# Performance work log

Hardware: AMD Instinct MI355X
Metric: run time of the kernel (lower is better)

The kernel has to match this reference:

```python
import jax, jax.numpy as jnp
import numpy as np

B, N, H, D = 1, 4096, 16, 64
C = H * D  # 1024
SCALE = D ** -0.5


def setup_inputs() -> dict:
    key = jax.random.key(0)
    k1, k2, k3, k4 = jax.random.split(key, 4)
    x = jax.random.normal(k1, (B, N, C), dtype=jnp.float32)
    # torch nn.Linear weights: [out_features, in_features]; y = x @ W.T + b
    w_qkv = jax.random.normal(k2, (3 * C, C), dtype=jnp.float32) * 0.02
    w_proj = jax.random.normal(k3, (C, C), dtype=jnp.float32) * 0.02
    b_proj = jax.random.normal(k4, (C,), dtype=jnp.float32) * 0.02
    return {"x": x, "w_qkv": w_qkv, "w_proj": w_proj, "b_proj": b_proj}


def reference(x, w_qkv, w_proj, b_proj):
    Bn, Nn, Cn = x.shape
    # fused QKV projection (no bias)
    qkv = jnp.einsum('bnc,oc->bno', x, w_qkv)            # [B,N,3C]
    qkv = qkv.reshape(Bn, Nn, 3, H, D)
    q = jnp.transpose(qkv[:, :, 0], (0, 2, 1, 3))        # [B,H,N,D]
    k = jnp.transpose(qkv[:, :, 1], (0, 2, 1, 3))
    v = jnp.transpose(qkv[:, :, 2], (0, 2, 1, 3))
    attn = jnp.einsum('bhnd,bhmd->bhnm', q, k) * SCALE   # [B,H,N,N]
    causal_mask = jnp.triu(jnp.ones((Nn, Nn), dtype=bool), k=1)
    attn = jnp.where(causal_mask, -jnp.inf, attn)
    attn = jax.nn.softmax(attn, axis=-1)
    out = jnp.einsum('bhnm,bhmd->bhnd', attn, v)          # [B,H,N,D]
    out = jnp.transpose(out, (0, 2, 1, 3)).reshape(Bn, Nn, Cn)
    out = jnp.einsum('bnc,oc->bno', out, w_proj) + b_proj
    return out
```

## Files before the change

kernel.cpp:

```cpp
#include <hip/hip_runtime.h>
#include <hip/hip_bf16.h>
#include <stdint.h>
#include <stddef.h>

using bf16 = __hip_bfloat16;
typedef short short8 __attribute__((ext_vector_type(8)));
typedef short short4v __attribute__((ext_vector_type(4)));
typedef short short2v __attribute__((ext_vector_type(2)));
typedef float f32x4 __attribute__((ext_vector_type(4)));
typedef float f32x16 __attribute__((ext_vector_type(16)));
typedef unsigned uintv4 __attribute__((ext_vector_type(4)));

#define MFMA16(A, B, C) __builtin_amdgcn_mfma_f32_16x16x32_bf16(A, B, C, 0, 0, 0)
#define MFMA32(A, B, C) __builtin_amdgcn_mfma_f32_32x32x16_bf16(A, B, C, 0, 0, 0)
#define GLOAD_LDS(g, l) __builtin_amdgcn_global_load_lds( \
    (const __attribute__((address_space(1))) void*)(g),   \
    (__attribute__((address_space(3))) void*)(l), 16, 0, 0)

constexpr int AN  = 4096;
constexpr int NH  = 16;
constexpr int HD  = 64;
constexpr int CC  = 1024;
constexpr int C3  = 3072;
constexpr float QSCALE = 0.125f * 1.4426950408889634f;

__device__ inline short bf16s(float f) {
    return (short)((__float_as_uint(f) + 0x8000u) >> 16);
}
__device__ inline float bf2f(short s) {
    return __uint_as_float(((unsigned)(unsigned short)s) << 16);
}
__device__ inline bf16 sbf(short s) {
    union { short s; bf16 b; } u;
    u.s = s;
    return u.b;
}
#if __has_builtin(__builtin_amdgcn_cvt_pk_bf16_f32)
typedef __bf16 bf16x2 __attribute__((ext_vector_type(2)));
__device__ inline short2v pk2(float a, float b) {
    bf16x2 r = __builtin_amdgcn_cvt_pk_bf16_f32(a, b);
    return *(short2v*)&r;
}
#else
__device__ inline short2v pk2(float a, float b) {
    unsigned ua = __float_as_uint(a) + 0x8000u;
    unsigned ub = __float_as_uint(b) + 0x8000u;
    unsigned r  = __builtin_amdgcn_perm(ub, ua, 0x07060302);
    return *(short2v*)&r;
}
#endif
__device__ inline unsigned pk2u(float a, float b) {
    short2v p = pk2(a, b);
    return *(unsigned*)&p;
}
__device__ inline short4v pack4(float a, float b, float c, float d) {
    short2v lo = pk2(a, b), hi = pk2(c, d);
    short4v r;
    r[0] = lo[0]; r[1] = lo[1]; r[2] = hi[0]; r[3] = hi[1];
    return r;
}
__device__ inline void plswap(unsigned &a, unsigned &b) {
    asm("v_permlane32_swap_b32 %0, %1" : "+v"(a), "+v"(b));
}
#if __has_builtin(__builtin_amdgcn_exp2f)
#define FAST_EXP2(x) __builtin_amdgcn_exp2f(x)
#else
#define FAST_EXP2(x) exp2f(x)
#endif

__device__ inline int detect_mode_inline(const unsigned short* xraw, int lane) {
    int crazy = 0;
    #pragma unroll
    for (int i = 0; i < 4; ++i) {
        const unsigned short u = xraw[lane * 4 + i];
        const int e = (u >> 7) & 0xFF;
        if (e >= 134 || (e != 0 && e <= 110)) ++crazy;
    }
    #pragma unroll
    for (int off = 32; off > 0; off >>= 1)
        crazy += __shfl_down(crazy, off, 64);
    crazy = __shfl(crazy, 0, 64);
    return (crazy >= 8) ? 1 : 0;
}

__device__ inline void cast8(const void* __restrict__ src,
                             bf16* __restrict__ dst, int i, int m) {
    if (m) {
        const float* s = (const float*)src;
        float4 a = *(const float4*)(s + i);
        float4 b = *(const float4*)(s + i + 4);
        short8 o;
        short2v p0 = pk2(a.x, a.y), p1 = pk2(a.z, a.w);
        short2v p2 = pk2(b.x, b.y), p3 = pk2(b.z, b.w);
        o[0] = p0[0]; o[1] = p0[1]; o[2] = p1[0]; o[3] = p1[1];
        o[4] = p2[0]; o[5] = p2[1]; o[6] = p3[0]; o[7] = p3[1];
        *(short8*)(dst + i) = o;
    } else {
        *(short8*)(dst + i) = *(const short8*)((const short*)src + i);
    }
}

__global__ void cast_all(const void* __restrict__ x, const void* __restrict__ wq,
                         const void* __restrict__ wp, const void* __restrict__ bp,
                         bf16* __restrict__ xb, bf16* __restrict__ wqb,
                         bf16* __restrict__ wpb, float* __restrict__ biasf,
                         int* __restrict__ mode) {
    const int b = blockIdx.x;
    const int tid = threadIdx.x;
    const int m = detect_mode_inline((const unsigned short*)x, tid & 63);
    if (b < 2048) {
        cast8(x, xb, (b * 256 + tid) * 8, m);
    } else if (b < 3584) {
        cast8(wq, wqb, ((b - 2048) * 256 + tid) * 8, m);
    } else if (b < 4096) {
        cast8(wp, wpb, ((b - 3584) * 256 + tid) * 8, m);
    } else {
        #pragma unroll
        for (int i = tid; i < CC; i += 256)
            biasf[i] = m ? ((const float*)bp)[i] : bf2f(((const short*)bp)[i]);
        if (tid == 0) *mode = m;
    }
}

constexpr int BM = 128, BN = 128, BK = 32;

__global__ __launch_bounds__(256, 3) void gemm_qkv(
    const bf16* __restrict__ A, const bf16* __restrict__ Bw,
    bf16* __restrict__ Cout, bf16* __restrict__ vTout)
{
    __shared__ bf16 As[BM * BK];
    __shared__ bf16 Bs[BN * BK];

    const int tid  = threadIdx.x;
    const int wave = tid >> 6;
    const int lane = tid & 63;
    const int quad = lane >> 4;
    const int l16  = lane & 15;
    const int wr   = wave >> 1;
    const int wc   = wave & 1;
    const int m0   = blockIdx.y * BM;
    const int o0   = blockIdx.x * BN;

    const int srow = lane >> 2;
    const int scol = (lane & 3) * 8;

    f32x4 acc[4][4] = {};

    for (int k0 = 0; k0 < CC; k0 += BK) {
        __syncthreads();
        #pragma unroll
        for (int c = 0; c < 2; ++c) {
            const int rbase = wave * 32 + c * 16;
            GLOAD_LDS(A + (size_t)(m0 + rbase + srow) * CC + k0 + scol, &As[rbase * BK]);
            GLOAD_LDS(Bw + (size_t)(o0 + rbase + srow) * CC + k0 + scol, &Bs[rbase * BK]);
        }
        __syncthreads();

        short8 af[4], bfr[4];
        #pragma unroll
        for (int i = 0; i < 4; ++i)
            af[i] = *(const short8*)&As[(wr * 64 + i * 16 + l16) * BK + quad * 8];
        #pragma unroll
        for (int j = 0; j < 4; ++j)
            bfr[j] = *(const short8*)&Bs[(wc * 64 + j * 16 + l16) * BK + quad * 8];
        #pragma unroll
        for (int i = 0; i < 4; ++i)
            #pragma unroll
            for (int j = 0; j < 4; ++j)
                acc[i][j] = MFMA16(af[i], bfr[j], acc[i][j]);
    }

    if (o0 >= 2 * CC) {
        #pragma unroll
        for (int j = 0; j < 4; ++j) {
            const int vc = o0 - 2 * CC + wc * 64 + j * 16 + l16;
            #pragma unroll
            for (int i = 0; i < 4; ++i) {
                const int row0 = m0 + wr * 64 + i * 16 + quad * 4;
                *(short4v*)&vTout[(size_t)vc * AN + row0] =
                    pack4(acc[i][j][0], acc[i][j][1], acc[i][j][2], acc[i][j][3]);
            }
        }
        return;
    }
    const float qs = (o0 < CC) ? QSCALE : 1.0f;
    #pragma unroll
    for (int j = 0; j < 4; ++j) {
        const int col = o0 + wc * 64 + j * 16 + l16;
        #pragma unroll
        for (int i = 0; i < 4; ++i) {
            const int row = m0 + wr * 64 + i * 16 + quad * 4;
            #pragma unroll
            for (int r = 0; r < 2; ++r) {
                short2v p = pk2(acc[i][j][2 * r] * qs, acc[i][j][2 * r + 1] * qs);
                Cout[(size_t)(row + 2 * r) * C3 + col]     = sbf(p[0]);
                Cout[(size_t)(row + 2 * r + 1) * C3 + col] = sbf(p[1]);
            }
        }
    }
}

constexpr int PM = 128, PN = 64, PK = 32;

__global__ __launch_bounds__(256, 2) void gemm_proj(
    const bf16* __restrict__ A, const bf16* __restrict__ Bw,
    const float* __restrict__ bias, void* __restrict__ Cout,
    const int* __restrict__ mode)
{
    __shared__ bf16 As[PM * PK];
    __shared__ bf16 Bs[PN * PK];

    const int tid  = threadIdx.x;
    const int wave = tid >> 6;
    const int lane = tid & 63;
    const int quad = lane >> 4;
    const int l16  = lane & 15;
    const int wr   = wave >> 1;
    const int wc   = wave & 1;
    const int m0   = blockIdx.y * PM;
    const int o0   = blockIdx.x * PN;
    const bool f32out = (*mode != 0);

    const int srow = lane >> 2;
    const int scol = (lane & 3) * 8;

    f32x4 acc[4][2] = {};

    for (int k0 = 0; k0 < CC; k0 += PK) {
        __syncthreads();
        #pragma unroll
        for (int c = 0; c < 2; ++c) {
            const int rbase = wave * 32 + c * 16;
            GLOAD_LDS(A + (size_t)(m0 + rbase + srow) * CC + k0 + scol, &As[rbase * PK]);
        }
        {
            const int rbase = wave * 16;
            GLOAD_LDS(Bw + (size_t)(o0 + rbase + srow) * CC + k0 + scol, &Bs[rbase * PK]);
        }
        __syncthreads();

        short8 af[4], bfr[2];
        #pragma unroll
        for (int i = 0; i < 4; ++i)
            af[i] = *(const short8*)&As[(wr * 64 + i * 16 + l16) * PK + quad * 8];
        #pragma unroll
        for (int j = 0; j < 2; ++j)
            bfr[j] = *(const short8*)&Bs[(wc * 32 + j * 16 + l16) * PK + quad * 8];
        #pragma unroll
        for (int i = 0; i < 4; ++i)
            #pragma unroll
            for (int j = 0; j < 2; ++j)
                acc[i][j] = MFMA16(af[i], bfr[j], acc[i][j]);
    }

    #pragma unroll
    for (int j = 0; j < 2; ++j) {
        const int col = o0 + wc * 32 + j * 16 + l16;
        const float bv = bias[col];
        #pragma unroll
        for (int i = 0; i < 4; ++i) {
            const int row = m0 + wr * 64 + i * 16 + quad * 4;
            if (f32out) {
                #pragma unroll
                for (int r = 0; r < 4; ++r)
                    ((float*)Cout)[(size_t)(row + r) * CC + col] = acc[i][j][r] + bv;
            } else {
                #pragma unroll
                for (int r = 0; r < 2; ++r) {
                    short2v p = pk2(acc[i][j][2 * r] + bv, acc[i][j][2 * r + 1] + bv);
                    ((bf16*)Cout)[(size_t)(row + 2 * r) * CC + col]     = sbf(p[0]);
                    ((bf16*)Cout)[(size_t)(row + 2 * r + 1) * CC + col] = sbf(p[1]);
                }
            }
        }
    }
}

constexpr int TK = 64;

__global__ __launch_bounds__(128, 2) void attn6(
    const bf16* __restrict__ qkv, const bf16* __restrict__ vT,
    bf16* __restrict__ pOn, float* __restrict__ pl)
{
    __shared__ bf16 Ks[2][TK * HD];
    __shared__ bf16 Vs[2][HD * TK];

    const int tid  = threadIdx.x;
    const int wave = tid >> 6;
    const int lane = tid & 63;
    const int l31  = lane & 31;
    const int hh   = lane >> 5;
    const int h7   = l31 & 7;
    const int h    = blockIdx.x & 15;
    const int t    = blockIdx.x >> 4;

    short8 ones8;
    #pragma unroll
    for (int i = 0; i < 8; ++i) ones8[i] = (short)0x3F80;

    const int sr  = lane >> 3;
    const int pc  = lane & 7;
    const int swz = pc ^ (sr & 7);

    #pragma unroll 1
    for (int pp = 0; pp < 2; ++pp) {
        const int tile = pp ? 63 - t : t;
        const int nIt  = tile + 1;
        const int i0   = pp ? ((64 - t) + 1) >> 1 : 0;
        const int i1   = pp ? 64 - t : (t + 2) >> 1;
        const int half = pp;
        const int qw   = tile * 64 + wave * 32;
        const int q    = qw + l31;

        short8 qf[4];
        {
            const bf16* qp = qkv + (size_t)q * C3 + h * HD + hh * 8;
            #pragma unroll
            for (int ki = 0; ki < 4; ++ki)
                qf[ki] = *(const short8*)(qp + ki * 16);
        }

        f32x16 acc_l = {};
        f32x16 acc_o[2] = {};

        if (i0 < i1) {
            const bf16 *kp[4], *vp[4];
            #pragma unroll
            for (int c = 0; c < 4; ++c) {
                const int row = wave * 32 + c * 8 + sr;
                kp[c] = qkv + (size_t)(i0 * TK + row) * C3 + CC + h * HD + swz * 8;
                vp[c] = vT + (size_t)(h * HD + row) * AN + i0 * TK + swz * 8;
            }
            auto stage = [&](int p) {
                #pragma unroll
                for (int c = 0; c < 4; ++c) {
                    const int rb = wave * 32 + c * 8;
                    GLOAD_LDS(kp[c], &Ks[p][rb * HD]);
                    GLOAD_LDS(vp[c], &Vs[p][rb * TK]);
                    kp[c] += (size_t)TK * C3;
                    vp[c] += TK;
                }
            };
            stage(0);
            __syncthreads();
            const bool hasdiag = (i1 == nIt);

            for (int it = i0; it < i1; ++it) {
                const int p = (it - i0) & 1;
                if (it + 1 < i1) stage(p ^ 1);

                f32x16 st[2];
                __builtin_amdgcn_s_setprio(1);
                #pragma unroll
                for (int kt = 0; kt < 2; ++kt) {
                    const int row = kt * 32 + l31;
                    f32x16 a = {};
                    #pragma unroll
                    for (int ki = 0; ki < 4; ++ki) {
                        short8 kf = *(const short8*)
                            &Ks[p][row * HD + (((2 * ki + hh) ^ h7) * 8)];
                        a = MFMA32(kf, qf[ki], a);
                    }
                    st[kt] = a;
                }
                __builtin_amdgcn_s_setprio(0);

                if (hasdiag && it == i1 - 1) {
                    const int kv0 = it * TK;
                    #pragma unroll
                    for (int kt = 0; kt < 2; ++kt)
                        #pragma unroll
                        for (int r = 0; r < 16; ++r) {
                            const int kv = kv0 + kt * 32 + (r & 3) + 8 * (r >> 2) + 4 * hh;
                            st[kt][r] = (kv <= q) ? FAST_EXP2(st[kt][r]) : 0.0f;
                        }
                } else {
                    #pragma unroll
                    for (int kt = 0; kt < 2; ++kt)
                        #pragma unroll
                        for (int r = 0; r < 16; ++r)
                            st[kt][r] = FAST_EXP2(st[kt][r]);
                }

                #pragma unroll
                for (int kt = 0; kt < 2; ++kt) {
                    #pragma unroll
                    for (int kc = 0; kc < 2; ++kc) {
                        unsigned a0 = pk2u(st[kt][kc * 8 + 0], st[kt][kc * 8 + 1]);
                        unsigned a1 = pk2u(st[kt][kc * 8 + 2], st[kt][kc * 8 + 3]);
                        unsigned c0 = pk2u(st[kt][kc * 8 + 4], st[kt][kc * 8 + 5]);
                        unsigned c1 = pk2u(st[kt][kc * 8 + 6], st[kt][kc * 8 + 7]);
                        plswap(a0, c0);
                        plswap(a1, c1);
                        uintv4 fu;
                        fu[0] = a0; fu[1] = a1; fu[2] = c0; fu[3] = c1;
                        const short8 frag = *(const short8*)&fu;

                        __builtin_amdgcn_s_setprio(1);
                        acc_l = MFMA32(ones8, frag, acc_l);
                        #pragma unroll
                        for (int dt2 = 0; dt2 < 2; ++dt2) {
                            const int row = dt2 * 32 + l31;
                            short8 vf = *(const short8*)
                                &Vs[p][row * TK + (((4 * kt + 2 * kc + hh) ^ h7) * 8)];
                            acc_o[dt2] = MFMA32(vf, frag, acc_o[dt2]);
                        }
                        __builtin_amdgcn_s_setprio(0);
                    }
                }
                __syncthreads();
            }
        }

        const size_t base = (size_t)half * AN * CC + (size_t)q * CC + h * HD;
        #pragma unroll
        for (int dt2 = 0; dt2 < 2; ++dt2)
            #pragma unroll
            for (int g = 0; g < 4; ++g) {
                const int d0 = dt2 * 32 + g * 8 + 4 * hh;
                *(short4v*)&pOn[base + d0] =
                    pack4(acc_o[dt2][4 * g + 0], acc_o[dt2][4 * g + 1],
                          acc_o[dt2][4 * g + 2], acc_o[dt2][4 * g + 3]);
            }
        if (hh == 0)
            pl[(size_t)half * NH * AN + (size_t)h * AN + q] = acc_l[0];
    }
}

__global__ __launch_bounds__(128) void combine_halves(
    const bf16* __restrict__ pOn, const float* __restrict__ pl,
    bf16* __restrict__ outp)
{
    const int q  = blockIdx.x;
    const int c0 = threadIdx.x * 8;
    const int h  = c0 >> 6;
    const float l0 = pl[(size_t)h * AN + q];
    const float l1 = pl[(size_t)NH * AN + (size_t)h * AN + q];
    const float L = l0 + l1;
    const float invL = (L > 0.f) ? 1.f / L : 0.f;
    const size_t off = (size_t)q * CC + c0;
    short8 o0 = *(const short8*)&pOn[off];
    short8 o1 = *(const short8*)&pOn[(size_t)AN * CC + off];
    short8 o;
    #pragma unroll
    for (int e = 0; e < 8; e += 2) {
        float v0 = (bf2f(o0[e])     + bf2f(o1[e]))     * invL;
        float v1 = (bf2f(o0[e + 1]) + bf2f(o1[e + 1])) * invL;
        short2v p = pk2(v0, v1);
        o[e] = p[0]; o[e + 1] = p[1];
    }
    *(short8*)&outp[off] = o;
}

extern "C" void kernel_launch(void* const* d_in, const int* in_sizes, int n_in,
                              void* d_out, int out_size, void* d_ws, size_t ws_size,
                              hipStream_t stream) {
    char* ws = (char*)d_ws;
    bf16*   qkv      = (bf16*)(ws);
    bf16*   attn_out = (bf16*)(ws + 25165824);
    bf16*   vT       = (bf16*)(ws + 33554432);
    bf16*   xb       = (bf16*)(ws + 41943040);
    bf16*   wqkvb    = (bf16*)(ws + 50331648);
    bf16*   wprojb   = (bf16*)(ws + 56623104);
    float*  biasf    = (float*)(ws + 58720256);
    int*    mode     = (int*)(ws + 58724352);
    bf16*   pOn      = (bf16*)(ws + 58728448);
    float*  pl       = (float*)(ws + 75505664);

    cast_all<<<dim3(4097), 256, 0, stream>>>(
        d_in[0], d_in[1], d_in[2], d_in[3], xb, wqkvb, wprojb, biasf, mode);

    gemm_qkv<<<dim3(C3 / BN, AN / BM), 256, 0, stream>>>(xb, wqkvb, qkv, vT);
    attn6<<<dim3(64 * NH), 128, 0, stream>>>(qkv, vT, pOn, pl);
    combine_halves<<<dim3(AN), 128, 0, stream>>>(pOn, pl, attn_out);
    gemm_proj<<<dim3(CC / PN, AN / PM), 256, 0, stream>>>(
        attn_out, wprojb, biasf, d_out, mode);
}
```

Baseline: 193.5 us.

## Split attention halves into separate blocks and restructure K/V staging pipeline

Each block now handles one of the two causal-balanced work halves, doubling the grid instead of looping over both halves. V loses its double buffer and is loaded just in time behind a mid-iteration barrier, while K stays double-buffered, and explicit vmcnt waits and scheduling barriers order the transfers. The row-sum MFMA against a ones vector is replaced by VALU accumulation plus one cross-lane shuffle. Launch bounds rise to 3 blocks per CU; the changes aim for more occupancy and fewer MFMA issues, at the cost of an extra barrier per iteration and less latency hiding for V loads.

```diff
diff --git a/kernel.cpp b/kernel.cpp
--- a/kernel.cpp
+++ b/kernel.cpp
@@ -278,12 +278,12 @@
 
 constexpr int TK = 64;
 
-__global__ __launch_bounds__(128, 2) void attn6(
+__global__ __launch_bounds__(128, 3) void attn7(
     const bf16* __restrict__ qkv, const bf16* __restrict__ vT,
     bf16* __restrict__ pOn, float* __restrict__ pl)
 {
     __shared__ bf16 Ks[2][TK * HD];
-    __shared__ bf16 Vs[2][HD * TK];
+    __shared__ bf16 Vs[HD * TK];
 
     const int tid  = threadIdx.x;
     const int wave = tid >> 6;
@@ -291,140 +291,169 @@
     const int l31  = lane & 31;
     const int hh   = lane >> 5;
     const int h7   = l31 & 7;
-    const int h    = blockIdx.x & 15;
-    const int t    = blockIdx.x >> 4;
-
-    short8 ones8;
-    #pragma unroll
-    for (int i = 0; i < 8; ++i) ones8[i] = (short)0x3F80;
+    const int bid  = blockIdx.x;
+    const int h    = bid & 15;
+    const int t    = (bid >> 4) & 63;
+    const int pp   = bid >> 10;
+
+    const int tile = pp ? 63 - t : t;
+    const int nIt  = tile + 1;
+    const int i0   = pp ? ((64 - t) + 1) >> 1 : 0;
+    const int i1   = pp ? 64 - t : (t + 2) >> 1;
+    const int half = pp;
+    const int qw   = tile * 64 + wave * 32;
+    const int q    = qw + l31;
 
     const int sr  = lane >> 3;
     const int pc  = lane & 7;
     const int swz = pc ^ (sr & 7);
 
-    #pragma unroll 1
-    for (int pp = 0; pp < 2; ++pp) {
-        const int tile = pp ? 63 - t : t;
-        const int nIt  = tile + 1;
-        const int i0   = pp ? ((64 - t) + 1) >> 1 : 0;
-        const int i1   = pp ? 64 - t : (t + 2) >> 1;
-        const int half = pp;
-        const int qw   = tile * 64 + wave * 32;
-        const int q    = qw + l31;
-
-        short8 qf[4];
-        {
-            const bf16* qp = qkv + (size_t)q * C3 + h * HD + hh * 8;
-            #pragma unroll
-            for (int ki = 0; ki < 4; ++ki)
-                qf[ki] = *(const short8*)(qp + ki * 16);
-        }
-
-        f32x16 acc_l = {};
-        f32x16 acc_o[2] = {};
-
-        if (i0 < i1) {
-            const bf16 *kp[4], *vp[4];
+    short8 qf[4];
+    {
+        const bf16* qp = qkv + (size_t)q * C3 + h * HD + hh * 8;
+        #pragma unroll
+        for (int ki = 0; ki < 4; ++ki)
+            qf[ki] = *(const short8*)(qp + ki * 16);
+    }
+
+    float lsum = 0.f;
+    f32x16 acc_o[2] = {};
+
+    if (i0 < i1) {
+        const bf16 *kp[4], *vp[4];
+        #pragma unroll
+        for (int c = 0; c < 4; ++c) {
+            const int row = wave * 32 + c * 8 + sr;
+            kp[c] = qkv + (size_t)(i0 * TK + row) * C3 + CC + h * HD + swz * 8;
+            vp[c] = vT + (size_t)(h * HD + row) * AN + i0 * TK + swz * 8;
+        }
+        auto stageK = [&](int buf) {
             #pragma unroll
             for (int c = 0; c < 4; ++c) {
-                const int row = wave * 32 + c * 8 + sr;
-                kp[c] = qkv + (size_t)(i0 * TK + row) * C3 + CC + h * HD + swz * 8;
-                vp[c] = vT + (size_t)(h * HD + row) * AN + i0 * TK + swz * 8;
-            }
-            auto stage = [&](int p) {
-                #pragma unroll
-                for (int c = 0; c < 4; ++c) {
-                    const int rb = wave * 32 + c * 8;
-                    GLOAD_LDS(kp[c], &Ks[p][rb * HD]);
-                    GLOAD_LDS(vp[c], &Vs[p][rb * TK]);
-                    kp[c] += (size_t)TK * C3;
-                    vp[c] += TK;
+                const int rb = wave * 32 + c * 8;
+                GLOAD_LDS(kp[c], &Ks[buf][rb * HD]);
+                kp[c] += (size_t)TK * C3;
+            }
+        };
+        auto stageV = [&]() {
+            #pragma unroll
+            for (int c = 0; c < 4; ++c) {
+                const int rb = wave * 32 + c * 8;
+                GLOAD_LDS(vp[c], &Vs[rb * TK]);
+                vp[c] += TK;
+            }
+        };
+
+        stageK(i0 & 1);
+        const bool hasdiag = (i1 == nIt);
+
+        for (int it = i0; it < i1; ++it) {
+            const int p = it & 1;
+            asm volatile("s_waitcnt vmcnt(0)" ::: "memory");
+            __builtin_amdgcn_s_barrier();
+            __builtin_amdgcn_sched_barrier(0);
+            stageV();
+            __builtin_amdgcn_sched_barrier(0);
+            const bool morek = (it + 1 < i1);
+            if (morek) stageK(p ^ 1);
+            __builtin_amdgcn_sched_barrier(0);
+
+            f32x16 st[2];
+            __builtin_amdgcn_s_setprio(1);
+            #pragma unroll
+            for (int kt = 0; kt < 2; ++kt) {
+                const int row = kt * 32 + l31;
+                f32x16 a = {};
+                #pragma unroll
+                for (int ki = 0; ki < 4; ++ki) {
+                    short8 kf = *(const short8*)
+                        &Ks[p][row * HD + (((2 * ki + hh) ^ h7) * 8)];
+                    a = MFMA32(kf, qf[ki], a);
                 }
-            };
-            stage(0);
-            __syncthreads();
-            const bool hasdiag = (i1 == nIt);
-
-            for (int it = i0; it < i1; ++it) {
-                const int p = (it - i0) & 1;
-                if (it + 1 < i1) stage(p ^ 1);
-
-                f32x16 st[2];
-                __builtin_amdgcn_s_setprio(1);
-                #pragma unroll
-                for (int kt = 0; kt < 2; ++kt) {
-                    const int row = kt * 32 + l31;
-                    f32x16 a = {};
+                st[kt] = a;
+            }
+            __builtin_amdgcn_s_setprio(0);
+
+            if (hasdiag && it == i1 - 1) {
+                const int kv0 = it * TK;
+                #pragma unroll
+                for (int kt = 0; kt < 2; ++kt)
                     #pragma unroll
-                    for (int ki = 0; ki < 4; ++ki) {
-                        short8 kf = *(const short8*)
-                            &Ks[p][row * HD + (((2 * ki + hh) ^ h7) * 8)];
-                        a = MFMA32(kf, qf[ki], a);
+                    for (int r = 0; r < 16; ++r) {
+                        const int kv = kv0 + kt * 32 + (r & 3) + 8 * (r >> 2) + 4 * hh;
+                        st[kt][r] = (kv <= q) ? FAST_EXP2(st[kt][r]) : 0.0f;
                     }
-                    st[kt] = a;
+            } else {
+                #pragma unroll
+                for (int kt = 0; kt < 2; ++kt)
+                    #pragma unroll
+                    for (int r = 0; r < 16; ++r)
+                        st[kt][r] = FAST_EXP2(st[kt][r]);
+            }
+
+            {
+                float s0 = 0.f, s1 = 0.f, s2 = 0.f, s3 = 0.f;
+                #pragma unroll
+                for (int kt = 0; kt < 2; ++kt)
+                    #pragma unroll
+                    for (int r = 0; r < 16; r += 4) {
+                        s0 += st[kt][r];     s1 += st[kt][r + 1];
+                        s2 += st[kt][r + 2]; s3 += st[kt][r + 3];
+                    }
+                lsum += (s0 + s1) + (s2 + s3);
+            }
+
+            short8 frag[2][2];
+            #pragma unroll
+            for (int kt = 0; kt < 2; ++kt)
+                #pragma unroll
+                for (int kc = 0; kc < 2; ++kc) {
+                    unsigned a0 = pk2u(st[kt][kc * 8 + 0], st[kt][kc * 8 + 1]);
+                    unsigned a1 = pk2u(st[kt][kc * 8 + 2], st[kt][kc * 8 + 3]);
+                    unsigned c0 = pk2u(st[kt][kc * 8 + 4], st[kt][kc * 8 + 5]);
+                    unsigned c1 = pk2u(st[kt][kc * 8 + 6], st[kt][kc * 8 + 7]);
+                    plswap(a0, c0);
+                    plswap(a1, c1);
+                    uintv4 fu;
+                    fu[0] = a0; fu[1] = a1; fu[2] = c0; fu[3] = c1;
+                    frag[kt][kc] = *(const short8*)&fu;
                 }
-                __builtin_amdgcn_s_setprio(0);
-
-                if (hasdiag && it == i1 - 1) {
-                    const int kv0 = it * TK;
+
+            if (morek) asm volatile("s_waitcnt vmcnt(4)" ::: "memory");
+            else       asm volatile("s_waitcnt vmcnt(0)" ::: "memory");
+            __builtin_amdgcn_s_barrier();
+            __builtin_amdgcn_sched_barrier(0);
+
+            __builtin_amdgcn_s_setprio(1);
+            #pragma unroll
+            for (int kt = 0; kt < 2; ++kt)
+                #pragma unroll
+                for (int kc = 0; kc < 2; ++kc) {
                     #pragma unroll
-                    for (int kt = 0; kt < 2; ++kt)
-                        #pragma unroll
-                        for (int r = 0; r < 16; ++r) {
-                            const int kv = kv0 + kt * 32 + (r & 3) + 8 * (r >> 2) + 4 * hh;
-                            st[kt][r] = (kv <= q) ? FAST_EXP2(st[kt][r]) : 0.0f;
-                        }
-                } else {
-                    #pragma unroll
-                    for (int kt = 0; kt < 2; ++kt)
-                        #pragma unroll
-                        for (int r = 0; r < 16; ++r)
-                            st[kt][r] = FAST_EXP2(st[kt][r]);
-                }
-
-                #pragma unroll
-                for (int kt = 0; kt < 2; ++kt) {
-                    #pragma unroll
-                    for (int kc = 0; kc < 2; ++kc) {
-                        unsigned a0 = pk2u(st[kt][kc * 8 + 0], st[kt][kc * 8 + 1]);
-                        unsigned a1 = pk2u(st[kt][kc * 8 + 2], st[kt][kc * 8 + 3]);
-                        unsigned c0 = pk2u(st[kt][kc * 8 + 4], st[kt][kc * 8 + 5]);
-                        unsigned c1 = pk2u(st[kt][kc * 8 + 6], st[kt][kc * 8 + 7]);
-                        plswap(a0, c0);
-                        plswap(a1, c1);
-                        uintv4 fu;
-                        fu[0] = a0; fu[1] = a1; fu[2] = c0; fu[3] = c1;
-                        const short8 frag = *(const short8*)&fu;
-
-                        __builtin_amdgcn_s_setprio(1);
-                        acc_l = MFMA32(ones8, frag, acc_l);
-                        #pragma unroll
-                        for (int dt2 = 0; dt2 < 2; ++dt2) {
-                            const int row = dt2 * 32 + l31;
-                            short8 vf = *(const short8*)
-                                &Vs[p][row * TK + (((4 * kt + 2 * kc + hh) ^ h7) * 8)];
-                            acc_o[dt2] = MFMA32(vf, frag, acc_o[dt2]);
-                        }
-                        __builtin_amdgcn_s_setprio(0);
+                    for (int dt2 = 0; dt2 < 2; ++dt2) {
+                        const int row = dt2 * 32 + l31;
+                        short8 vf = *(const short8*)
+                            &Vs[row * TK + (((4 * kt + 2 * kc + hh) ^ h7) * 8)];
+                        acc_o[dt2] = MFMA32(vf, frag[kt][kc], acc_o[dt2]);
                     }
                 }
-                __syncthreads();
-            }
-        }
-
-        const size_t base = (size_t)half * AN * CC + (size_t)q * CC + h * HD;
-        #pragma unroll
-        for (int dt2 = 0; dt2 < 2; ++dt2)
-            #pragma unroll
-            for (int g = 0; g < 4; ++g) {
-                const int d0 = dt2 * 32 + g * 8 + 4 * hh;
-                *(short4v*)&pOn[base + d0] =
-                    pack4(acc_o[dt2][4 * g + 0], acc_o[dt2][4 * g + 1],
-                          acc_o[dt2][4 * g + 2], acc_o[dt2][4 * g + 3]);
-            }
-        if (hh == 0)
-            pl[(size_t)half * NH * AN + (size_t)h * AN + q] = acc_l[0];
-    }
+            __builtin_amdgcn_s_setprio(0);
+        }
+    }
+
+    const size_t base = (size_t)half * AN * CC + (size_t)q * CC + h * HD;
+    #pragma unroll
+    for (int dt2 = 0; dt2 < 2; ++dt2)
+        #pragma unroll
+        for (int g = 0; g < 4; ++g) {
+            const int d0 = dt2 * 32 + g * 8 + 4 * hh;
+            *(short4v*)&pOn[base + d0] =
+                pack4(acc_o[dt2][4 * g + 0], acc_o[dt2][4 * g + 1],
+                      acc_o[dt2][4 * g + 2], acc_o[dt2][4 * g + 3]);
+        }
+    const float ltot = lsum + __shfl_xor(lsum, 32, 64);
+    if (hh == 0)
+        pl[(size_t)half * NH * AN + (size_t)h * AN + q] = ltot;
 }
 
 __global__ __launch_bounds__(128) void combine_halves(
@@ -471,7 +500,7 @@
         d_in[0], d_in[1], d_in[2], d_in[3], xb, wqkvb, wprojb, biasf, mode);
 
     gemm_qkv<<<dim3(C3 / BN, AN / BM), 256, 0, stream>>>(xb, wqkvb, qkv, vT);
-    attn6<<<dim3(64 * NH), 128, 0, stream>>>(qkv, vT, pOn, pl);
+    attn7<<<dim3(64 * NH * 2), 128, 0, stream>>>(qkv, vT, pOn, pl);
     combine_halves<<<dim3(AN), 128, 0, stream>>>(pOn, pl, attn_out);
     gemm_proj<<<dim3(CC / PN, AN / PM), 256, 0, stream>>>(
         attn_out, wprojb, biasf, d_out, mode);
```

After: 197.4 us. Within noise of the previous version (+2.0%).

## Pack K and V in fragment order and load attention operands directly to registers

Applied to the files above, without the earlier changes.

The QKV GEMM now writes Q, K and V to separate buffers, with K and V stored in a per-head, per-64-row-tile layout that matches the MFMA fragment order. The attention kernel drops its LDS staging and __syncthreads, loading K and V fragments straight from global memory into registers and prefetching the next K tile. This removes LDS traffic and block barriers, but each wave in a block now fetches the same K/V data independently from global/L2 with no LDS sharing. It also raises register pressure, and the K epilogue now does scattered scalar stores.

```diff
diff --git a/kernel.cpp b/kernel.cpp
--- a/kernel.cpp
+++ b/kernel.cpp
@@ -126,7 +126,7 @@
 
 __global__ __launch_bounds__(256, 3) void gemm_qkv(
     const bf16* __restrict__ A, const bf16* __restrict__ Bw,
-    bf16* __restrict__ Cout, bf16* __restrict__ vTout)
+    bf16* __restrict__ qOut, bf16* __restrict__ kOut, bf16* __restrict__ vOut)
 {
     __shared__ bf16 As[BM * BK];
     __shared__ bf16 Bs[BN * BK];
@@ -173,17 +173,36 @@
     if (o0 >= 2 * CC) {
         #pragma unroll
         for (int j = 0; j < 4; ++j) {
-            const int vc = o0 - 2 * CC + wc * 64 + j * 16 + l16;
+            const int dcol = o0 - 2 * CC + wc * 64 + j * 16 + l16;
+            const int hV = dcol >> 6, dV = dcol & 63;
             #pragma unroll
             for (int i = 0; i < 4; ++i) {
-                const int row0 = m0 + wr * 64 + i * 16 + quad * 4;
-                *(short4v*)&vTout[(size_t)vc * AN + row0] =
+                const int kv0 = m0 + wr * 64 + i * 16 + quad * 4;
+                const size_t addr = (size_t)hV * 64 * AN + (size_t)(kv0 >> 6) * 4096
+                                  + (size_t)((kv0 >> 3) & 7) * 512 + dV * 8 + (kv0 & 7);
+                *(short4v*)&vOut[addr] =
                     pack4(acc[i][j][0], acc[i][j][1], acc[i][j][2], acc[i][j][3]);
             }
         }
         return;
     }
-    const float qs = (o0 < CC) ? QSCALE : 1.0f;
+    if (o0 >= CC) {
+        #pragma unroll
+        for (int j = 0; j < 4; ++j) {
+            const int dcol = o0 - CC + wc * 64 + j * 16 + l16;
+            const int hK = dcol >> 6, dc = (dcol >> 3) & 7, de = dcol & 7;
+            #pragma unroll
+            for (int i = 0; i < 4; ++i) {
+                const int kv0 = m0 + wr * 64 + i * 16 + quad * 4;
+                const size_t addr = (size_t)hK * 64 * AN + (size_t)(kv0 >> 6) * 4096
+                                  + (size_t)dc * 512 + (size_t)(kv0 & 63) * 8 + de;
+                #pragma unroll
+                for (int r = 0; r < 4; ++r)
+                    kOut[addr + r * 8] = sbf(bf16s(acc[i][j][r]));
+            }
+        }
+        return;
+    }
     #pragma unroll
     for (int j = 0; j < 4; ++j) {
         const int col = o0 + wc * 64 + j * 16 + l16;
@@ -192,9 +211,9 @@
             const int row = m0 + wr * 64 + i * 16 + quad * 4;
             #pragma unroll
             for (int r = 0; r < 2; ++r) {
-                short2v p = pk2(acc[i][j][2 * r] * qs, acc[i][j][2 * r + 1] * qs);
-                Cout[(size_t)(row + 2 * r) * C3 + col]     = sbf(p[0]);
-                Cout[(size_t)(row + 2 * r + 1) * C3 + col] = sbf(p[1]);
+                short2v p = pk2(acc[i][j][2 * r] * QSCALE, acc[i][j][2 * r + 1] * QSCALE);
+                qOut[(size_t)(row + 2 * r) * CC + col]     = sbf(p[0]);
+                qOut[(size_t)(row + 2 * r + 1) * CC + col] = sbf(p[1]);
             }
         }
     }
@@ -278,19 +297,14 @@
 
 constexpr int TK = 64;
 
-__global__ __launch_bounds__(128, 2) void attn6(
-    const bf16* __restrict__ qkv, const bf16* __restrict__ vT,
-    bf16* __restrict__ pOn, float* __restrict__ pl)
+__global__ __launch_bounds__(128, 2) void attn8(
+    const bf16* __restrict__ qbuf, const bf16* __restrict__ kP,
+    const bf16* __restrict__ vP, bf16* __restrict__ pOn, float* __restrict__ pl)
 {
-    __shared__ bf16 Ks[2][TK * HD];
-    __shared__ bf16 Vs[2][HD * TK];
-
     const int tid  = threadIdx.x;
-    const int wave = tid >> 6;
     const int lane = tid & 63;
     const int l31  = lane & 31;
     const int hh   = lane >> 5;
-    const int h7   = l31 & 7;
     const int h    = blockIdx.x & 15;
     const int t    = blockIdx.x >> 4;
 
@@ -298,9 +312,6 @@
     #pragma unroll
     for (int i = 0; i < 8; ++i) ones8[i] = (short)0x3F80;
 
-    const int sr  = lane >> 3;
-    const int pc  = lane & 7;
-    const int swz = pc ^ (sr & 7);
 
     #pragma unroll 1
     for (int pp = 0; pp < 2; ++pp) {
@@ -309,12 +320,12 @@
         const int i0   = pp ? ((64 - t) + 1) >> 1 : 0;
         const int i1   = pp ? 64 - t : (t + 2) >> 1;
         const int half = pp;
-        const int qw   = tile * 64 + wave * 32;
+        const int qw   = tile * 64 + (tid >> 6) * 32;
         const int q    = qw + l31;
 
         short8 qf[4];
         {
-            const bf16* qp = qkv + (size_t)q * C3 + h * HD + hh * 8;
+            const bf16* qp = qbuf + (size_t)q * CC + h * HD + hh * 8;
             #pragma unroll
             for (int ki = 0; ki < 4; ++ki)
                 qf[ki] = *(const short8*)(qp + ki * 16);
@@ -324,46 +335,50 @@
         f32x16 acc_o[2] = {};
 
         if (i0 < i1) {
-            const bf16 *kp[4], *vp[4];
-            #pragma unroll
-            for (int c = 0; c < 4; ++c) {
-                const int row = wave * 32 + c * 8 + sr;
-                kp[c] = qkv + (size_t)(i0 * TK + row) * C3 + CC + h * HD + swz * 8;
-                vp[c] = vT + (size_t)(h * HD + row) * AN + i0 * TK + swz * 8;
-            }
-            auto stage = [&](int p) {
-                #pragma unroll
-                for (int c = 0; c < 4; ++c) {
-                    const int rb = wave * 32 + c * 8;
-                    GLOAD_LDS(kp[c], &Ks[p][rb * HD]);
-                    GLOAD_LDS(vp[c], &Vs[p][rb * TK]);
-                    kp[c] += (size_t)TK * C3;
-                    vp[c] += TK;
-                }
-            };
-            stage(0);
-            __syncthreads();
+            const bf16* kb = kP + (size_t)h * 64 * AN + (size_t)i0 * 4096;
+            const bf16* vb = vP + (size_t)h * 64 * AN + (size_t)i0 * 4096;
             const bool hasdiag = (i1 == nIt);
 
+            short8 kf[8];
+            #pragma unroll
+            for (int kt = 0; kt < 2; ++kt)
+                #pragma unroll
+                for (int ki = 0; ki < 4; ++ki)
+                    kf[kt * 4 + ki] = *(const short8*)
+                        (kb + (2 * ki + hh) * 512 + kt * 256 + l31 * 8);
+            kb += 4096;
+
             for (int it = i0; it < i1; ++it) {
-                const int p = (it - i0) & 1;
-                if (it + 1 < i1) stage(p ^ 1);
+                short8 vf[8];
+                #pragma unroll
+                for (int kk = 0; kk < 4; ++kk)
+                    #pragma unroll
+                    for (int dt2 = 0; dt2 < 2; ++dt2)
+                        vf[kk * 2 + dt2] = *(const short8*)
+                            (vb + (2 * kk + hh) * 512 + dt2 * 256 + l31 * 8);
+                vb += 4096;
 
                 f32x16 st[2];
                 __builtin_amdgcn_s_setprio(1);
                 #pragma unroll
                 for (int kt = 0; kt < 2; ++kt) {
-                    const int row = kt * 32 + l31;
                     f32x16 a = {};
                     #pragma unroll
-                    for (int ki = 0; ki < 4; ++ki) {
-                        short8 kf = *(const short8*)
-                            &Ks[p][row * HD + (((2 * ki + hh) ^ h7) * 8)];
-                        a = MFMA32(kf, qf[ki], a);
-                    }
+                    for (int ki = 0; ki < 4; ++ki)
+                        a = MFMA32(kf[kt * 4 + ki], qf[ki], a);
                     st[kt] = a;
                 }
                 __builtin_amdgcn_s_setprio(0);
+
+                if (it + 1 < i1) {
+                    #pragma unroll
+                    for (int kt = 0; kt < 2; ++kt)
+                        #pragma unroll
+                        for (int ki = 0; ki < 4; ++ki)
+                            kf[kt * 4 + ki] = *(const short8*)
+                                (kb + (2 * ki + hh) * 512 + kt * 256 + l31 * 8);
+                    kb += 4096;
+                }
 
                 if (hasdiag && it == i1 - 1) {
                     const int kv0 = it * TK;
@@ -383,7 +398,7 @@
                 }
 
                 #pragma unroll
-                for (int kt = 0; kt < 2; ++kt) {
+                for (int kt = 0; kt < 2; ++kt)
                     #pragma unroll
                     for (int kc = 0; kc < 2; ++kc) {
                         unsigned a0 = pk2u(st[kt][kc * 8 + 0], st[kt][kc * 8 + 1]);
@@ -399,16 +414,11 @@
                         __builtin_amdgcn_s_setprio(1);
                         acc_l = MFMA32(ones8, frag, acc_l);
                         #pragma unroll
-                        for (int dt2 = 0; dt2 < 2; ++dt2) {
-                            const int row = dt2 * 32 + l31;
-                            short8 vf = *(const short8*)
-                                &Vs[p][row * TK + (((4 * kt + 2 * kc + hh) ^ h7) * 8)];
-                            acc_o[dt2] = MFMA32(vf, frag, acc_o[dt2]);
-                        }
+                        for (int dt2 = 0; dt2 < 2; ++dt2)
+                            acc_o[dt2] = MFMA32(vf[(kt * 2 + kc) * 2 + dt2],
+                                                frag, acc_o[dt2]);
                         __builtin_amdgcn_s_setprio(0);
                     }
-                }
-                __syncthreads();
             }
         }
 
@@ -456,22 +466,24 @@
                               void* d_out, int out_size, void* d_ws, size_t ws_size,
                               hipStream_t stream) {
     char* ws = (char*)d_ws;
-    bf16*   qkv      = (bf16*)(ws);
+    bf16*   qbuf     = (bf16*)(ws);
+    bf16*   kPack    = (bf16*)(ws + 8388608);
+    bf16*   vPack    = (bf16*)(ws + 16777216);
     bf16*   attn_out = (bf16*)(ws + 25165824);
-    bf16*   vT       = (bf16*)(ws + 33554432);
-    bf16*   xb       = (bf16*)(ws + 41943040);
-    bf16*   wqkvb    = (bf16*)(ws + 50331648);
-    bf16*   wprojb   = (bf16*)(ws + 56623104);
-    float*  biasf    = (float*)(ws + 58720256);
-    int*    mode     = (int*)(ws + 58724352);
-    bf16*   pOn      = (bf16*)(ws + 58728448);
-    float*  pl       = (float*)(ws + 75505664);
+    bf16*   xb       = (bf16*)(ws + 33554432);
+    bf16*   wqkvb    = (bf16*)(ws + 41943040);
+    bf16*   wprojb   = (bf16*)(ws + 48234496);
+    float*  biasf    = (float*)(ws + 50331648);
+    int*    mode     = (int*)(ws + 50335744);
+    bf16*   pOn      = (bf16*)(ws + 50339840);
+    float*  pl       = (float*)(ws + 67117056);
 
     cast_all<<<dim3(4097), 256, 0, stream>>>(
         d_in[0], d_in[1], d_in[2], d_in[3], xb, wqkvb, wprojb, biasf, mode);
 
-    gemm_qkv<<<dim3(C3 / BN, AN / BM), 256, 0, stream>>>(xb, wqkvb, qkv, vT);
-    attn6<<<dim3(64 * NH), 128, 0, stream>>>(qkv, vT, pOn, pl);
+    gemm_qkv<<<dim3(C3 / BN, AN / BM), 256, 0, stream>>>(
+        xb, wqkvb, qbuf, kPack, vPack);
+    attn8<<<dim3(64 * NH), 128, 0, stream>>>(qbuf, kPack, vPack, pOn, pl);
     combine_halves<<<dim3(AN), 128, 0, stream>>>(pOn, pl, attn_out);
     gemm_proj<<<dim3(CC / PN, AN / PM), 256, 0, stream>>>(
         attn_out, wprojb, biasf, d_out, mode);
```

Result: slower. 200.0 us (+3.4%).
